# Optimization experiments

Hardware: AMD Instinct MI355X
Metric: run time of the kernel (lower is better)

## Reference

```python
import jax, jax.numpy as jnp
import numpy as np

B, C, IMG, P = 8, 6, 384, 16
DIM, HEADS, DEPTH, MLP, NCLS = 768, 12, 4, 3072, 1000
N = (IMG // P) ** 2            # 576 patches
DH = DIM // HEADS              # 64
PATCH_DIM = C * P * P          # 1536


def setup_inputs() -> dict:
    key = jax.random.key(0)
    ks = jax.random.split(key, 13)
    f = lambda k, shp, s=0.02: jax.random.normal(k, shp, jnp.float32) * s
    return {
        "x": jax.random.normal(ks[0], (B, C, IMG, IMG), jnp.float32),
        "patch_w": f(ks[1], (PATCH_DIM, DIM)),
        "patch_b": f(ks[2], (DIM,)),
        "ln1_g": jnp.ones((DEPTH, DIM), jnp.float32),
        "ln1_b": jnp.zeros((DEPTH, DIM), jnp.float32),
        "w_qkv": f(ks[3], (DEPTH, DIM, 3 * DIM)),
        "bias_att": f(ks[4], (DEPTH, HEADS, N, N), 0.5),
        "w_out": f(ks[5], (DEPTH, DIM, DIM)),
        "ln2_g": jnp.ones((DEPTH, DIM), jnp.float32),
        "ln2_b": jnp.zeros((DEPTH, DIM), jnp.float32),
        "w1": f(ks[6], (DEPTH, DIM, MLP)),
        "b1": f(ks[7], (DEPTH, MLP)),
        "w2": f(ks[8], (DEPTH, MLP, DIM)),
        "b2": f(ks[9], (DEPTH, DIM)),
        "lnh_g": jnp.ones((DIM,), jnp.float32),
        "lnh_b": jnp.zeros((DIM,), jnp.float32),
        "w_head": f(ks[10], (DIM, NCLS)),
        "b_head": f(ks[11], (NCLS,)),
    }


def _ln(x, g, b, eps=1e-5):
    m = x.mean(-1, keepdims=True)
    v = ((x - m) ** 2).mean(-1, keepdims=True)
    return (x - m) * jax.lax.rsqrt(v + eps) * g + b


def _patchify(x, patch_w, patch_b):
    # Rearrange 'b c (h p1) (w p2) -> b (h w) (p1 p2 c)' then Linear(patch_dim, dim)
    b = x.shape[0]
    g = IMG // P
    x = x.reshape(b, C, g, P, g, P).transpose(0, 2, 4, 3, 5, 1).reshape(b, g * g, PATCH_DIM)
    return x @ patch_w + patch_b


def _forward(x, patch_w, patch_b, ln1_g, ln1_b, w_qkv, bias_att, w_out,
             ln2_g, ln2_b, w1, b1, w2, b2, lnh_g, lnh_b, w_head, b_head):
    scale = DH ** -0.5
    tok = _patchify(x, patch_w, patch_b)  # [B, N, DIM]; pos_info='mul_att_normed' -> no pos_embed added

    def block(t, p):
        l1g, l1b, wqkv, bias, wout, l2g, l2b, ww1, bb1, ww2, bb2 = p
        h = _ln(t, l1g, l1b)
        qkv = h @ wqkv                                     # [B, N, 3*DIM]
        q, k, v = jnp.split(qkv, 3, axis=-1)
        rs = lambda a: a.reshape(t.shape[0], N, HEADS, DH).transpose(0, 2, 1, 3)
        q, k, v = rs(q), rs(k), rs(v)                      # [B, H, N, DH]
        dots = jnp.einsum('bhid,bhjd->bhij', q, k) * scale
        # mul_att_normed: softmax(qk) * softmax(bias), renormalized over keys
        attn = jax.nn.softmax(dots, axis=-1) * jax.nn.softmax(bias, axis=-1)[None]
        attn = attn / attn.sum(-1, keepdims=True)
        o = jnp.einsum('bhij,bhjd->bhid', attn, v)
        o = o.transpose(0, 2, 1, 3).reshape(t.shape[0], N, DIM) @ wout
        t = t + o
        h2 = _ln(t, l2g, l2b)
        t = t + (jax.nn.gelu(h2 @ ww1 + bb1, approximate=False) @ ww2 + bb2)
        return t, None

    tok, _ = jax.lax.scan(block, tok,
                          (ln1_g, ln1_b, w_qkv, bias_att, w_out,
                           ln2_g, ln2_b, w1, b1, w2, b2))
    pooled = tok.mean(axis=1)                              # mean-pool tokens
    return _ln(pooled, lnh_g, lnh_b) @ w_head + b_head     # [B, NCLS]


def reference(x, patch_w, patch_b, ln1_g, ln1_b, w_qkv, bias_att, w_out,
              ln2_g, ln2_b, w1, b1, w2, b2, lnh_g, lnh_b, w_head, b_head):
    return _forward(x, patch_w, patch_b, ln1_g, ln1_b, w_qkv, bias_att, w_out,
                    ln2_g, ln2_b, w1, b1, w2, b2, lnh_g, lnh_b, w_head, b_head)
```

## Files before the change

kernel.cpp:

```cpp
#include <hip/hip_runtime.h>
#include <hip/hip_bf16.h>

typedef __attribute__((ext_vector_type(8))) short bf16x8;
typedef __attribute__((ext_vector_type(4))) float f32x4;

#define DEVI __device__ __forceinline__

DEVI unsigned short f2bf_bits(float f) {
    __hip_bfloat16 h = __float2bfloat16(f);
    return *reinterpret_cast<unsigned short*>(&h);
}
DEVI float bfbits2f(unsigned short u) {
    __hip_bfloat16 h = *reinterpret_cast<__hip_bfloat16*>(&u);
    return __bfloat162float(h);
}

DEVI void gload_lds16(const void* g, void* lds) {
    __builtin_amdgcn_global_load_lds(
        (const __attribute__((address_space(1))) unsigned int*)g,
        (__attribute__((address_space(3))) unsigned int*)lds, 16, 0, 0);
}

template <int N> DEVI void wait_vm() {
    if constexpr (N == 0) asm volatile("s_waitcnt vmcnt(0)" ::: "memory");
    else if constexpr (N == 6) asm volatile("s_waitcnt vmcnt(6)" ::: "memory");
    else if constexpr (N == 12) asm volatile("s_waitcnt vmcnt(12)" ::: "memory");
    __builtin_amdgcn_sched_barrier(0);
}

DEVI int2 remap2d(int bid, int total, int gx) {
    int q = total >> 3, r = total & 7, x = bid & 7, l = bid >> 3;
    int seq = (x < r ? x * (q + 1) : r * (q + 1) + (x - r) * q) + l;
    int g4 = seq / (4 * gx);
    int rem = seq - g4 * 4 * gx;
    return {g4 * 4 + (rem & 3), rem >> 2};
}

__global__ __launch_bounds__(256) void patchify_kernel(const float* __restrict__ x,
                                                       unsigned short* __restrict__ patches)
{
    size_t t8 = (size_t)blockIdx.x * 256 + threadIdx.x;
    int jq = (int)(t8 % 48);
    size_t t = t8 / 48;
    int r = (int)(t % 384); t /= 384;
    int c = (int)(t % 6);
    int b = (int)(t / 6);
    int j = jq * 8;
    int gh = r >> 4, p1 = r & 15, gw = j >> 4, p2 = j & 15;
    int prow = b * 576 + gh * 24 + gw;
    int pcol = c * 256 + p1 * 16 + p2;
    const float* src = x + ((((size_t)b * 6 + c) * 384 + r) * 384 + j);
    float4 v0 = ((const float4*)src)[0];
    float4 v1 = ((const float4*)src)[1];
    ushort u[8] = { f2bf_bits(v0.x), f2bf_bits(v0.y), f2bf_bits(v0.z), f2bf_bits(v0.w),
                    f2bf_bits(v1.x), f2bf_bits(v1.y), f2bf_bits(v1.z), f2bf_bits(v1.w) };
    *(int4*)&patches[(size_t)prow * 1536 + pcol] = *(int4*)u;
}

__global__ __launch_bounds__(256) void convT_patch_kernel(const float* __restrict__ W,
                                                          __hip_bfloat16* __restrict__ Wt)
{
    __shared__ float tile[32][33];
    int n0 = blockIdx.x * 32, kp0 = blockIdx.y * 32;
    int tx = threadIdx.x & 31, ty = threadIdx.x >> 5;
#pragma unroll
    for (int i = 0; i < 4; i++) {
        int kp = kp0 + ty + 8 * i;
        int k = (kp & 255) * 6 + (kp >> 8);
        tile[ty + 8 * i][tx] = W[(size_t)k * 768 + n0 + tx];
    }
    __syncthreads();
#pragma unroll
    for (int i = 0; i < 4; i++)
        Wt[(size_t)(n0 + ty + 8 * i) * 1536 + kp0 + tx] = __float2bfloat16(tile[tx][ty + 8 * i]);
}

DEVI void convT_body(const float* __restrict__ W, __hip_bfloat16* __restrict__ Wt,
                     int K, int N, int k0, int n0, int tid)
{
    __shared__ float tile[32][33];
    int tx = tid & 31, ty = tid >> 5;
#pragma unroll
    for (int i = 0; i < 4; i++)
        tile[ty + 8 * i][tx] = W[(size_t)(k0 + ty + 8 * i) * N + n0 + tx];
    __syncthreads();
#pragma unroll
    for (int i = 0; i < 4; i++)
        Wt[(size_t)(n0 + ty + 8 * i) * K + k0 + tx] = __float2bfloat16(tile[tx][ty + 8 * i]);
}

__global__ __launch_bounds__(256) void convT4_kernel(const float* __restrict__ wqkv,
                                                     const float* __restrict__ wout,
                                                     const float* __restrict__ w1,
                                                     const float* __restrict__ w2,
                                                     __hip_bfloat16* __restrict__ dst)
{
    int bt = blockIdx.x;
    const float* W; __hip_bfloat16* Wt; int K, N, lt;
    if (bt < 1728)      { W = wqkv; K = 768;  N = 2304; lt = bt;        Wt = dst; }
    else if (bt < 2304) { W = wout; K = 768;  N = 768;  lt = bt - 1728; Wt = dst + 1769472; }
    else if (bt < 4608) { W = w1;   K = 768;  N = 3072; lt = bt - 2304; Wt = dst + 2359296; }
    else                { W = w2;   K = 3072; N = 768;  lt = bt - 4608; Wt = dst + 4718592; }
    int tn = N >> 5;
    convT_body(W, Wt, K, N, (lt / tn) * 32, (lt % tn) * 32, threadIdx.x);
}

DEVI float ld_ln(const float* p) { return *p; }
DEVI float ld_ln(const __hip_bfloat16* p) { return __bfloat162float(*p); }
DEVI void st_ln(float* p, float v) { *p = v; }
DEVI void st_ln(__hip_bfloat16* p, float v) { *p = __float2bfloat16(v); }

template <typename InT, typename OutT>
__global__ __launch_bounds__(256) void ln_kernel(const InT* __restrict__ x,
                                                 const float* __restrict__ g,
                                                 const float* __restrict__ b,
                                                 OutT* __restrict__ out)
{
    int row = blockIdx.x, tid = threadIdx.x;
    const InT* xr = x + (size_t)row * 768;
    float v0 = ld_ln(&xr[tid]), v1 = ld_ln(&xr[tid + 256]), v2 = ld_ln(&xr[tid + 512]);
    float s = v0 + v1 + v2;
    float s2 = v0 * v0 + v1 * v1 + v2 * v2;
#pragma unroll
    for (int m = 32; m >= 1; m >>= 1) { s += __shfl_xor(s, m); s2 += __shfl_xor(s2, m); }
    __shared__ float red[8];
    int w = tid >> 6;
    if ((tid & 63) == 0) { red[w] = s; red[4 + w] = s2; }
    __syncthreads();
    s = red[0] + red[1] + red[2] + red[3];
    s2 = red[4] + red[5] + red[6] + red[7];
    float mean = s * (1.0f / 768.0f);
    float var = s2 * (1.0f / 768.0f) - mean * mean;
    float rstd = rsqrtf(var + 1e-5f);
    OutT* orow = out + (size_t)row * 768;
    st_ln(&orow[tid], (v0 - mean) * rstd * g[tid] + b[tid]);
    st_ln(&orow[tid + 256], (v1 - mean) * rstd * g[tid + 256] + b[tid + 256]);
    st_ln(&orow[tid + 512], (v2 - mean) * rstd * g[tid + 512] + b[tid + 512]);
}

template <bool BIAS, bool RESID>
__global__ __launch_bounds__(256, 2) void gemm_bt_kernel(
    const __hip_bfloat16* __restrict__ A,
    const __hip_bfloat16* __restrict__ Bt,
    const float* __restrict__ bias,
    const __hip_bfloat16* __restrict__ resid,
    __hip_bfloat16* __restrict__ Cb,
    int M, int N, int K, int gx)
{
    constexpr int BM = 64, SL = 6;
    __shared__ __align__(16) __hip_bfloat16 As[3][BM * 64];
    __shared__ __align__(16) __hip_bfloat16 Bs[3][128 * 64];
    const int tid = threadIdx.x;
    const int wid = tid >> 6, lane = tid & 63;
    const int g = lane >> 4, l16 = lane & 15;
    const int wm = (wid >> 1) * 32, wn = (wid & 1) * 64;

    int2 bc = remap2d(blockIdx.x, gridDim.x, gx);
    const int bm = bc.x * BM, bn = bc.y * 128;

    const int sr32 = tid >> 3, ci = tid & 7;
    const int cg = ci ^ (sr32 & 7);
    const int sdst = tid * 8;
    size_t aOff[2], bOff[4];
#pragma unroll
    for (int i = 0; i < 2; i++) aOff[i] = (size_t)(bm + i * 32 + sr32) * K + cg * 8;
#pragma unroll
    for (int i = 0; i < 4; i++) bOff[i] = (size_t)(bn + i * 32 + sr32) * K + cg * 8;

    auto stage = [&](__hip_bfloat16* asb, __hip_bfloat16* bsb, int tq) {
        const __hip_bfloat16* ap = A + tq * 64;
        const __hip_bfloat16* bp = Bt + tq * 64;
#pragma unroll
        for (int i = 0; i < 2; i++) gload_lds16(ap + aOff[i], asb + i * 2048 + sdst);
#pragma unroll
        for (int i = 0; i < 4; i++) gload_lds16(bp + bOff[i], bsb + i * 2048 + sdst);
    };

    f32x4 acc[2][4] = {};
    const int nt = K >> 6;

    stage(As[0], Bs[0], 0);
    stage(As[1], Bs[1], 1);
    stage(As[2], Bs[2], 2);
    wait_vm<2 * SL>();
    __builtin_amdgcn_s_barrier();
    __builtin_amdgcn_sched_barrier(0);

    for (int t = 0; t < nt; t += 3) {
#pragma unroll
        for (int u = 0; u < 3; u++) {
            const int tc = t + u;
            bf16x8 af[2][2], bfr[2][4];
#pragma unroll
            for (int s = 0; s < 2; s++) {
                const int cp = ((s * 4 + g) ^ (l16 & 7)) << 3;
#pragma unroll
                for (int mi = 0; mi < 2; mi++)
                    af[s][mi] = *(const bf16x8*)&As[u][(wm + mi * 16 + l16) * 64 + cp];
#pragma unroll
                for (int ni = 0; ni < 4; ni++)
                    bfr[s][ni] = *(const bf16x8*)&Bs[u][(wn + ni * 16 + l16) * 64 + cp];
            }
#pragma unroll
            for (int s = 0; s < 2; s++)
#pragma unroll
                for (int mi = 0; mi < 2; mi++)
#pragma unroll
                    for (int ni = 0; ni < 4; ni++)
                        acc[mi][ni] = __builtin_amdgcn_mfma_f32_16x16x32_bf16(af[s][mi], bfr[s][ni], acc[mi][ni], 0, 0, 0);

            asm volatile("s_waitcnt lgkmcnt(0)" ::: "memory");
            __builtin_amdgcn_sched_barrier(0);
            __builtin_amdgcn_s_barrier();
            __builtin_amdgcn_sched_barrier(0);

            if (tc + 3 < nt) stage(As[u], Bs[u], tc + 3);
            if (tc + 1 < nt) {
                if (tc + 4 <= nt)      wait_vm<2 * SL>();
                else if (tc + 3 == nt) wait_vm<SL>();
                else                   wait_vm<0>();
                __builtin_amdgcn_s_barrier();
                __builtin_amdgcn_sched_barrier(0);
            }
        }
    }

    __hip_bfloat16* scr = &As[0][0] + wid * (16 * 72);
#pragma unroll
    for (int mi = 0; mi < 2; mi++) {
#pragma unroll
        for (int ni = 0; ni < 4; ni++) {
            float bval = 0.0f;
            if (BIAS) bval = bias[bn + wn + ni * 16 + l16];
#pragma unroll
            for (int r = 0; r < 4; r++)
                scr[(4 * g + r) * 72 + ni * 16 + l16] = __float2bfloat16(acc[mi][ni][r] + bval);
        }
        asm volatile("s_waitcnt lgkmcnt(0)" ::: "memory");
        __builtin_amdgcn_sched_barrier(0);
#pragma unroll
        for (int q2 = 0; q2 < 2; q2++) {
            int row16 = q2 * 8 + (lane >> 3), ch = lane & 7;
            bf16x8 vv = *(const bf16x8*)&scr[row16 * 72 + ch * 8];
            int grow = bm + wm + mi * 16 + row16;
            size_t off = (size_t)grow * N + bn + wn + ch * 8;
            if (RESID) {
                bf16x8 rv = *(const bf16x8*)&resid[off];
#pragma unroll
                for (int e = 0; e < 8; e++)
                    vv[e] = (short)f2bf_bits(bfbits2f((unsigned short)vv[e]) + bfbits2f((unsigned short)rv[e]));
            }
            *(int4*)&Cb[off] = *(int4*)&vv;
        }
        asm volatile("s_waitcnt lgkmcnt(0)" ::: "memory");
        __builtin_amdgcn_sched_barrier(0);
    }
}

template <bool BIAS, bool GELU>
__global__ __launch_bounds__(256, 2) void gemm_wide_kernel(
    const __hip_bfloat16* __restrict__ A,
    const __hip_bfloat16* __restrict__ Bt,
    const float* __restrict__ bias,
    __hip_bfloat16* __restrict__ Cb,
    int M, int N, int K, int gx)
{
    constexpr int SL = 6;
    __shared__ __align__(16) __hip_bfloat16 As[3][128 * 32];
    __shared__ __align__(16) __hip_bfloat16 Bs[3][256 * 32];
    const int tid = threadIdx.x;
    const int wid = tid >> 6, lane = tid & 63;
    const int g = lane >> 4, l16 = lane & 15;
    const int wm = (wid >> 1) * 64, wn = (wid & 1) * 128;

    int2 bc = remap2d(blockIdx.x, gridDim.x, gx);
    const int bm = bc.x * 128, bn = bc.y * 256;

    const int sr = tid >> 2;
    const int csrc = (lane & 3) ^ ((lane >> 3) & 3);
    const int sdst = sr * 32 + (lane & 3) * 8;
    size_t aOff[2], bOff[4];
#pragma unroll
    for (int i = 0; i < 2; i++) aOff[i] = (size_t)(bm + i * 64 + sr) * K + csrc * 8;
#pragma unroll
    for (int i = 0; i < 4; i++) bOff[i] = (size_t)(bn + i * 64 + sr) * K + csrc * 8;

    auto stage = [&](__hip_bfloat16* asb, __hip_bfloat16* bsb, int tq) {
        const __hip_bfloat16* ap = A + tq * 32;
        const __hip_bfloat16* bp = Bt + tq * 32;
#pragma unroll
        for (int i = 0; i < 2; i++) gload_lds16(ap + aOff[i], asb + i * 2048 + sdst);
#pragma unroll
        for (int i = 0; i < 4; i++) gload_lds16(bp + bOff[i], bsb + i * 2048 + sdst);
    };

    const int pSw = (l16 >> 1) & 3;
    f32x4 acc[4][8] = {};
    const int nt = K >> 5;

    stage(As[0], Bs[0], 0);
    stage(As[1], Bs[1], 1);
    stage(As[2], Bs[2], 2);
    wait_vm<2 * SL>();
    __builtin_amdgcn_s_barrier();
    __builtin_amdgcn_sched_barrier(0);

    for (int t = 0; t < nt; t += 3) {
#pragma unroll
        for (int u = 0; u < 3; u++) {
            const int tc = t + u;
            bf16x8 af[4], bfr[8];
#pragma unroll
            for (int mi = 0; mi < 4; mi++)
                af[mi] = *(const bf16x8*)&As[u][(wm + mi * 16 + l16) * 32 + ((g ^ pSw) << 3)];
#pragma unroll
            for (int ni = 0; ni < 8; ni++)
                bfr[ni] = *(const bf16x8*)&Bs[u][(wn + ni * 16 + l16) * 32 + ((g ^ pSw) << 3)];
#pragma unroll
            for (int mi = 0; mi < 4; mi++)
#pragma unroll
                for (int ni = 0; ni < 8; ni++)
                    acc[mi][ni] = __builtin_amdgcn_mfma_f32_16x16x32_bf16(af[mi], bfr[ni], acc[mi][ni], 0, 0, 0);

            asm volatile("s_waitcnt lgkmcnt(0)" ::: "memory");
            __builtin_amdgcn_sched_barrier(0);
            __builtin_amdgcn_s_barrier();
            __builtin_amdgcn_sched_barrier(0);

            if (tc + 3 < nt) stage(As[u], Bs[u], tc + 3);
            if (tc + 1 < nt) {
                if (tc + 4 <= nt)      wait_vm<2 * SL>();
                else if (tc + 3 == nt) wait_vm<SL>();
                else                   wait_vm<0>();
                __builtin_amdgcn_s_barrier();
                __builtin_amdgcn_sched_barrier(0);
            }
        }
    }

    __hip_bfloat16* scr = &As[0][0] + wid * (16 * 136);
#pragma unroll
    for (int mi = 0; mi < 4; mi++) {
#pragma unroll
        for (int ni = 0; ni < 8; ni++) {
            float bval = 0.0f;
            if (BIAS) bval = bias[bn + wn + ni * 16 + l16];
#pragma unroll
            for (int r = 0; r < 4; r++) {
                float v = acc[mi][ni][r] + bval;
                if (GELU) v = 0.5f * v * (1.0f + erff(v * 0.70710678118654752f));
                scr[(4 * g + r) * 136 + ni * 16 + l16] = __float2bfloat16(v);
            }
        }
        asm volatile("s_waitcnt lgkmcnt(0)" ::: "memory");
        __builtin_amdgcn_sched_barrier(0);
#pragma unroll
        for (int q2 = 0; q2 < 4; q2++) {
            int idx = q2 * 64 + lane;
            int row16 = idx >> 4, ch = idx & 15;
            bf16x8 vv = *(const bf16x8*)&scr[row16 * 136 + ch * 8];
            int grow = bm + wm + mi * 16 + row16;
            *(int4*)&Cb[(size_t)grow * N + bn + wn + ch * 8] = *(int4*)&vv;
        }
        asm volatile("s_waitcnt lgkmcnt(0)" ::: "memory");
        __builtin_amdgcn_sched_barrier(0);
    }
}

__global__ __launch_bounds__(256) void attn_kernel(const __hip_bfloat16* __restrict__ qkvb,
                                                   const float* __restrict__ bias,
                                                   unsigned short* __restrict__ o)
{
    const int seq = (blockIdx.x & 7) * 108 + (blockIdx.x >> 3);
    const int bb = seq & 7, qt = (seq >> 3) % 9, h = seq / 72;
    const int q0 = qt * 64;
    const int tid = threadIdx.x;
    const int wq = tid >> 6, lane = tid & 63, g = lane >> 4, l16 = lane & 15;

    __shared__ __align__(16) unsigned short Qs[64 * 72];
    __shared__ __align__(16) unsigned short Ks[64 * 72];
    __shared__ __align__(16) unsigned short Vt[64 * 72];
    __shared__ __align__(16) unsigned short Ps[4][16 * 72];

    {
        int r = tid >> 2, cb = (tid & 3) * 16;
        const int4* s4 = (const int4*)&qkvb[(size_t)(bb * 576 + q0 + r) * 2304 + h * 64 + cb];
        int4* d4 = (int4*)&Qs[r * 72 + cb];
        d4[0] = s4[0]; d4[1] = s4[1];
    }
    __syncthreads();
    bf16x8 qf0 = *(const bf16x8*)&Qs[(wq * 16 + l16) * 72 + g * 8];
    bf16x8 qf1 = *(const bf16x8*)&Qs[(wq * 16 + l16) * 72 + 32 + g * 8];

    float m_r[4] = {-1e30f, -1e30f, -1e30f, -1e30f};
    float l_r[4] = {0.f, 0.f, 0.f, 0.f};
    f32x4 oa[4] = {};
    const float* bias_h = bias + (size_t)h * 576 * 576;
    const float scale = 0.125f;

    for (int kt = 0; kt < 576; kt += 64) {
        {
            int r = tid >> 2, cb = (tid & 3) * 16;
            const int4* s4 = (const int4*)&qkvb[(size_t)(bb * 576 + kt + r) * 2304 + 768 + h * 64 + cb];
            int4* d4 = (int4*)&Ks[r * 72 + cb];
            d4[0] = s4[0]; d4[1] = s4[1];
            int key = tid & 63, d0 = (tid >> 6) * 16;
            const unsigned short* vs = (const unsigned short*)&qkvb[(size_t)(bb * 576 + kt + key) * 2304 + 1536 + h * 64 + d0];
            bf16x8 v0 = *(const bf16x8*)vs;
            bf16x8 v1 = *(const bf16x8*)(vs + 8);
#pragma unroll
            for (int e = 0; e < 8; e++) {
                Vt[(d0 + e) * 72 + key] = (unsigned short)v0[e];
                Vt[(d0 + 8 + e) * 72 + key] = (unsigned short)v1[e];
            }
        }
        __syncthreads();

        float bl[4][4];
#pragma unroll
        for (int kc = 0; kc < 4; kc++)
#pragma unroll
            for (int r = 0; r < 4; r++) {
                int q = q0 + wq * 16 + 4 * g + r;
                bl[kc][r] = bias_h[(size_t)q * 576 + kt + kc * 16 + l16];
            }

        f32x4 sc[4] = {};
        __builtin_amdgcn_s_setprio(1);
#pragma unroll
        for (int kc = 0; kc < 4; kc++) {
            bf16x8 kf0 = *(const bf16x8*)&Ks[(kc * 16 + l16) * 72 + g * 8];
            bf16x8 kf1 = *(const bf16x8*)&Ks[(kc * 16 + l16) * 72 + 32 + g * 8];
            sc[kc] = __builtin_amdgcn_mfma_f32_16x16x32_bf16(qf0, kf0, sc[kc], 0, 0, 0);
            sc[kc] = __builtin_amdgcn_mfma_f32_16x16x32_bf16(qf1, kf1, sc[kc], 0, 0, 0);
        }
        __builtin_amdgcn_s_setprio(0);

        float sv[4][4], mt[4] = {-1e30f, -1e30f, -1e30f, -1e30f};
#pragma unroll
        for (int kc = 0; kc < 4; kc++)
#pragma unroll
            for (int r = 0; r < 4; r++) {
                float s = sc[kc][r] * scale + bl[kc][r];
                sv[kc][r] = s;
                mt[r] = fmaxf(mt[r], s);
            }
#pragma unroll
        for (int r = 0; r < 4; r++)
#pragma unroll
            for (int m = 1; m < 16; m <<= 1) mt[r] = fmaxf(mt[r], __shfl_xor(mt[r], m));

        float sf[4];
#pragma unroll
        for (int r = 0; r < 4; r++) {
            float mn = fmaxf(m_r[r], mt[r]);
            sf[r] = __expf(m_r[r] - mn);
            m_r[r] = mn;
        }
        float rs[4] = {0.f, 0.f, 0.f, 0.f};
#pragma unroll
        for (int kc = 0; kc < 4; kc++)
#pragma unroll
            for (int r = 0; r < 4; r++) {
                float p = __expf(sv[kc][r] - m_r[r]);
                rs[r] += p;
                Ps[wq][(4 * g + r) * 72 + kc * 16 + l16] = f2bf_bits(p);
            }
#pragma unroll
        for (int r = 0; r < 4; r++) {
#pragma unroll
            for (int m = 1; m < 16; m <<= 1) rs[r] += __shfl_xor(rs[r], m);
            l_r[r] = l_r[r] * sf[r] + rs[r];
        }
#pragma unroll
        for (int dt = 0; dt < 4; dt++)
#pragma unroll
            for (int r = 0; r < 4; r++) oa[dt][r] *= sf[r];

        asm volatile("s_waitcnt lgkmcnt(0)" ::: "memory");

        __builtin_amdgcn_s_setprio(1);
#pragma unroll
        for (int s = 0; s < 2; s++) {
            bf16x8 pf = *(const bf16x8*)&Ps[wq][l16 * 72 + s * 32 + g * 8];
#pragma unroll
            for (int dt = 0; dt < 4; dt++) {
                bf16x8 vf = *(const bf16x8*)&Vt[(dt * 16 + l16) * 72 + s * 32 + g * 8];
                oa[dt] = __builtin_amdgcn_mfma_f32_16x16x32_bf16(pf, vf, oa[dt], 0, 0, 0);
            }
        }
        __builtin_amdgcn_s_setprio(0);
        __syncthreads();
    }

#pragma unroll
    for (int dt = 0; dt < 4; dt++)
#pragma unroll
        for (int r = 0; r < 4; r++) {
            int q = q0 + wq * 16 + 4 * g + r;
            float v = oa[dt][r] / l_r[r];
            o[(size_t)(bb * 576 + q) * 768 + h * 64 + dt * 16 + l16] = f2bf_bits(v);
        }
}

__global__ __launch_bounds__(256) void pool_kernel(const __hip_bfloat16* __restrict__ tok,
                                                   float* __restrict__ pooled)
{
    int d = blockIdx.x * 256 + threadIdx.x;
    int b = blockIdx.y;
    float s = 0.0f;
    for (int n = 0; n < 576; n++) s += __bfloat162float(tok[(size_t)(b * 576 + n) * 768 + d]);
    pooled[b * 768 + d] = s * (1.0f / 576.0f);
}

__global__ __launch_bounds__(256) void head_kernel(const float* __restrict__ lnp,
                                                   const float* __restrict__ w,
                                                   const float* __restrict__ bh,
                                                   float* __restrict__ out)
{
    int c = blockIdx.x * 256 + threadIdx.x;
    int b = blockIdx.y;
    if (c >= 1000) return;
    float s = bh[c];
    for (int d = 0; d < 768; d++) s += lnp[b * 768 + d] * w[(size_t)d * 1000 + c];
    out[b * 1000 + c] = s;
}

extern "C" void kernel_launch(void* const* d_in, const int* in_sizes, int n_in,
                              void* d_out, int out_size, void* d_ws, size_t ws_size,
                              hipStream_t stream)
{
    const float* x = (const float*)d_in[0];
    const float* patch_w = (const float*)d_in[1];
    const float* patch_b = (const float*)d_in[2];
    const float* ln1_g = (const float*)d_in[3];
    const float* ln1_b = (const float*)d_in[4];
    const float* w_qkv = (const float*)d_in[5];
    const float* bias_att = (const float*)d_in[6];
    const float* w_out = (const float*)d_in[7];
    const float* ln2_g = (const float*)d_in[8];
    const float* ln2_b = (const float*)d_in[9];
    const float* w1 = (const float*)d_in[10];
    const float* b1 = (const float*)d_in[11];
    const float* w2 = (const float*)d_in[12];
    const float* b2 = (const float*)d_in[13];
    const float* lnh_g = (const float*)d_in[14];
    const float* lnh_b = (const float*)d_in[15];
    const float* w_head = (const float*)d_in[16];
    const float* b_head = (const float*)d_in[17];
    float* out = (float*)d_out;

    char* ws = (char*)d_ws;
    __hip_bfloat16* tok = (__hip_bfloat16*)(ws + 0);
    __hip_bfloat16* qkv_bf = (__hip_bfloat16*)(ws + 14155776);
    float* pooled = (float*)(ws + 56623104);
    float* pooledln = (float*)(ws + 56647680);
    __hip_bfloat16* patches = (__hip_bfloat16*)(ws + 56672256);
    __hip_bfloat16* lw = patches;
    __hip_bfloat16* h_bf = (__hip_bfloat16*)(ws + 70828032);
    __hip_bfloat16* o_bf = (__hip_bfloat16*)(ws + 77905920);
    __hip_bfloat16* hid_bf = (__hip_bfloat16*)(ws + 84983808);
    __hip_bfloat16* wbuf = (__hip_bfloat16*)(ws + 113295360);

    patchify_kernel<<<3456, 256, 0, stream>>>(x, (unsigned short*)patches);
    convT_patch_kernel<<<dim3(24, 48), 256, 0, stream>>>(patch_w, wbuf);
    gemm_bt_kernel<true, false><<<432, 256, 0, stream>>>(
        patches, wbuf, patch_b, nullptr, tok, 4608, 768, 1536, 6);

    for (int l = 0; l < 4; l++) {
        convT4_kernel<<<6912, 256, 0, stream>>>(
            w_qkv + (size_t)l * 768 * 2304, w_out + (size_t)l * 768 * 768,
            w1 + (size_t)l * 768 * 3072, w2 + (size_t)l * 3072 * 768, lw);
        ln_kernel<__hip_bfloat16, __hip_bfloat16><<<4608, 256, 0, stream>>>(
            tok, ln1_g + l * 768, ln1_b + l * 768, h_bf);
        gemm_wide_kernel<false, false><<<324, 256, 0, stream>>>(
            h_bf, lw, nullptr, qkv_bf, 4608, 2304, 768, 9);
        attn_kernel<<<864, 256, 0, stream>>>(
            qkv_bf, bias_att + (size_t)l * 12 * 576 * 576, (unsigned short*)o_bf);
        gemm_bt_kernel<false, true><<<432, 256, 0, stream>>>(
            o_bf, lw + 1769472, nullptr, tok, tok, 4608, 768, 768, 6);
        ln_kernel<__hip_bfloat16, __hip_bfloat16><<<4608, 256, 0, stream>>>(
            tok, ln2_g + l * 768, ln2_b + l * 768, h_bf);
        gemm_wide_kernel<true, true><<<432, 256, 0, stream>>>(
            h_bf, lw + 2359296, b1 + l * 3072, hid_bf, 4608, 3072, 768, 12);
        gemm_bt_kernel<true, true><<<432, 256, 0, stream>>>(
            hid_bf, lw + 4718592, b2 + l * 768, tok, tok, 4608, 768, 3072, 6);
    }

    pool_kernel<<<dim3(3, 8), 256, 0, stream>>>(tok, pooled);
    ln_kernel<float, float><<<8, 256, 0, stream>>>(pooled, lnh_g, lnh_b, pooledln);
    head_kernel<<<dim3(4, 8), 256, 0, stream>>>(pooledln, w_head, b_head, out);
}
```

Measured before the change: 845.4 us.

## Replace wide GEMM with 64x128 tiles, batch weight conversion, vectorize LayerNorm

Removes the 128x256-tile wide GEMM and runs the QKV and MLP-up projections through the smaller 64x128 tile kernel, which gains a GELU template flag. The smaller tiles give more blocks (1296 and 1728) to fill the CUs, at the cost of less data reuse per block. When the workspace is large enough, all four layers' weights are transposed and converted in a single launch instead of one launch per layer. LayerNorm now runs 192 threads per row with float4/ushort4 vector loads and stores.

```diff
diff --git a/kernel.cpp b/kernel.cpp
--- a/kernel.cpp
+++ b/kernel.cpp
@@ -25,6 +25,10 @@
     if constexpr (N == 0) asm volatile("s_waitcnt vmcnt(0)" ::: "memory");
     else if constexpr (N == 6) asm volatile("s_waitcnt vmcnt(6)" ::: "memory");
     else if constexpr (N == 12) asm volatile("s_waitcnt vmcnt(12)" ::: "memory");
+    __builtin_amdgcn_sched_barrier(0);
+}
+DEVI void lgkm0() {
+    asm volatile("s_waitcnt lgkmcnt(0)" ::: "memory");
     __builtin_amdgcn_sched_barrier(0);
 }
 
@@ -89,56 +93,85 @@
         Wt[(size_t)(n0 + ty + 8 * i) * K + k0 + tx] = __float2bfloat16(tile[tx][ty + 8 * i]);
 }
 
-__global__ __launch_bounds__(256) void convT4_kernel(const float* __restrict__ wqkv,
-                                                     const float* __restrict__ wout,
-                                                     const float* __restrict__ w1,
-                                                     const float* __restrict__ w2,
-                                                     __hip_bfloat16* __restrict__ dst)
-{
-    int bt = blockIdx.x;
+DEVI void convT4_dispatch(int bt, const float* wqkv, const float* wout,
+                          const float* w1, const float* w2,
+                          __hip_bfloat16* dst, int tid)
+{
     const float* W; __hip_bfloat16* Wt; int K, N, lt;
     if (bt < 1728)      { W = wqkv; K = 768;  N = 2304; lt = bt;        Wt = dst; }
     else if (bt < 2304) { W = wout; K = 768;  N = 768;  lt = bt - 1728; Wt = dst + 1769472; }
     else if (bt < 4608) { W = w1;   K = 768;  N = 3072; lt = bt - 2304; Wt = dst + 2359296; }
     else                { W = w2;   K = 3072; N = 768;  lt = bt - 4608; Wt = dst + 4718592; }
     int tn = N >> 5;
-    convT_body(W, Wt, K, N, (lt / tn) * 32, (lt % tn) * 32, threadIdx.x);
-}
-
-DEVI float ld_ln(const float* p) { return *p; }
-DEVI float ld_ln(const __hip_bfloat16* p) { return __bfloat162float(*p); }
-DEVI void st_ln(float* p, float v) { *p = v; }
-DEVI void st_ln(__hip_bfloat16* p, float v) { *p = __float2bfloat16(v); }
+    convT_body(W, Wt, K, N, (lt / tn) * 32, (lt % tn) * 32, tid);
+}
+
+__global__ __launch_bounds__(256) void convT4_kernel(const float* __restrict__ wqkv,
+                                                     const float* __restrict__ wout,
+                                                     const float* __restrict__ w1,
+                                                     const float* __restrict__ w2,
+                                                     __hip_bfloat16* __restrict__ dst)
+{
+    convT4_dispatch(blockIdx.x, wqkv, wout, w1, w2, dst, threadIdx.x);
+}
+
+__global__ __launch_bounds__(256) void convT4all_kernel(const float* __restrict__ wqkv,
+                                                        const float* __restrict__ wout,
+                                                        const float* __restrict__ w1,
+                                                        const float* __restrict__ w2,
+                                                        __hip_bfloat16* __restrict__ dst)
+{
+    int l = blockIdx.x / 6912, bt = blockIdx.x % 6912;
+    convT4_dispatch(bt,
+                    wqkv + (size_t)l * 768 * 2304, wout + (size_t)l * 768 * 768,
+                    w1 + (size_t)l * 768 * 3072, w2 + (size_t)l * 3072 * 768,
+                    dst + (size_t)l * 7077888, threadIdx.x);
+}
+
+DEVI void ld4(const float* p, float* v) {
+    float4 t = *(const float4*)p; v[0] = t.x; v[1] = t.y; v[2] = t.z; v[3] = t.w;
+}
+DEVI void ld4(const __hip_bfloat16* p, float* v) {
+    ushort4 t = *(const ushort4*)p;
+    v[0] = bfbits2f(t.x); v[1] = bfbits2f(t.y); v[2] = bfbits2f(t.z); v[3] = bfbits2f(t.w);
+}
+DEVI void st4(float* p, const float* v) { *(float4*)p = make_float4(v[0], v[1], v[2], v[3]); }
+DEVI void st4(__hip_bfloat16* p, const float* v) {
+    ushort4 t = { f2bf_bits(v[0]), f2bf_bits(v[1]), f2bf_bits(v[2]), f2bf_bits(v[3]) };
+    *(ushort4*)p = t;
+}
 
 template <typename InT, typename OutT>
-__global__ __launch_bounds__(256) void ln_kernel(const InT* __restrict__ x,
+__global__ __launch_bounds__(192) void ln_kernel(const InT* __restrict__ x,
                                                  const float* __restrict__ g,
                                                  const float* __restrict__ b,
                                                  OutT* __restrict__ out)
 {
     int row = blockIdx.x, tid = threadIdx.x;
-    const InT* xr = x + (size_t)row * 768;
-    float v0 = ld_ln(&xr[tid]), v1 = ld_ln(&xr[tid + 256]), v2 = ld_ln(&xr[tid + 512]);
-    float s = v0 + v1 + v2;
-    float s2 = v0 * v0 + v1 * v1 + v2 * v2;
+    float v[4], gv[4], bv[4];
+    ld4(&x[(size_t)row * 768 + tid * 4], v);
+    float s = v[0] + v[1] + v[2] + v[3];
+    float s2 = v[0] * v[0] + v[1] * v[1] + v[2] * v[2] + v[3] * v[3];
 #pragma unroll
     for (int m = 32; m >= 1; m >>= 1) { s += __shfl_xor(s, m); s2 += __shfl_xor(s2, m); }
-    __shared__ float red[8];
+    __shared__ float red[6];
     int w = tid >> 6;
-    if ((tid & 63) == 0) { red[w] = s; red[4 + w] = s2; }
+    if ((tid & 63) == 0) { red[w] = s; red[3 + w] = s2; }
     __syncthreads();
-    s = red[0] + red[1] + red[2] + red[3];
-    s2 = red[4] + red[5] + red[6] + red[7];
+    s = red[0] + red[1] + red[2];
+    s2 = red[3] + red[4] + red[5];
     float mean = s * (1.0f / 768.0f);
     float var = s2 * (1.0f / 768.0f) - mean * mean;
     float rstd = rsqrtf(var + 1e-5f);
-    OutT* orow = out + (size_t)row * 768;
-    st_ln(&orow[tid], (v0 - mean) * rstd * g[tid] + b[tid]);
-    st_ln(&orow[tid + 256], (v1 - mean) * rstd * g[tid + 256] + b[tid + 256]);
-    st_ln(&orow[tid + 512], (v2 - mean) * rstd * g[tid + 512] + b[tid + 512]);
-}
-
-template <bool BIAS, bool RESID>
+    ld4(&g[tid * 4], gv);
+    ld4(&b[tid * 4], bv);
+    float o[4];
+#pragma unroll
+    for (int i = 0; i < 4; i++) o[i] = (v[i] - mean) * rstd * gv[i] + bv[i];
+    st4(&out[(size_t)row * 768 + tid * 4], o);
+}
+
+template <bool BIAS, bool RESID, bool GELU>
 __global__ __launch_bounds__(256, 2) void gemm_bt_kernel(
     const __hip_bfloat16* __restrict__ A,
     const __hip_bfloat16* __restrict__ Bt,
@@ -182,7 +215,7 @@
     stage(As[0], Bs[0], 0);
     stage(As[1], Bs[1], 1);
     stage(As[2], Bs[2], 2);
-    wait_vm<2 * SL>();
+    wait_vm<12>();
     __builtin_amdgcn_s_barrier();
     __builtin_amdgcn_sched_barrier(0);
 
@@ -209,15 +242,14 @@
                     for (int ni = 0; ni < 4; ni++)
                         acc[mi][ni] = __builtin_amdgcn_mfma_f32_16x16x32_bf16(af[s][mi], bfr[s][ni], acc[mi][ni], 0, 0, 0);
 
-            asm volatile("s_waitcnt lgkmcnt(0)" ::: "memory");
-            __builtin_amdgcn_sched_barrier(0);
+            lgkm0();
             __builtin_amdgcn_s_barrier();
             __builtin_amdgcn_sched_barrier(0);
 
             if (tc + 3 < nt) stage(As[u], Bs[u], tc + 3);
             if (tc + 1 < nt) {
-                if (tc + 4 <= nt)      wait_vm<2 * SL>();
-                else if (tc + 3 == nt) wait_vm<SL>();
+                if (tc + 4 <= nt)      wait_vm<12>();
+                else if (tc + 3 == nt) wait_vm<6>();
                 else                   wait_vm<0>();
                 __builtin_amdgcn_s_barrier();
                 __builtin_amdgcn_sched_barrier(0);
@@ -233,11 +265,13 @@
             float bval = 0.0f;
             if (BIAS) bval = bias[bn + wn + ni * 16 + l16];
 #pragma unroll
-            for (int r = 0; r < 4; r++)
-                scr[(4 * g + r) * 72 + ni * 16 + l16] = __float2bfloat16(acc[mi][ni][r] + bval);
-        }
-        asm volatile("s_waitcnt lgkmcnt(0)" ::: "memory");
-        __builtin_amdgcn_sched_barrier(0);
+            for (int r = 0; r < 4; r++) {
+                float v = acc[mi][ni][r] + bval;
+                if (GELU) v = 0.5f * v * (1.0f + erff(v * 0.70710678118654752f));
+                scr[(4 * g + r) * 72 + ni * 16 + l16] = __float2bfloat16(v);
+            }
+        }
+        lgkm0();
 #pragma unroll
         for (int q2 = 0; q2 < 2; q2++) {
             int row16 = q2 * 8 + (lane >> 3), ch = lane & 7;
@@ -252,118 +286,7 @@
             }
             *(int4*)&Cb[off] = *(int4*)&vv;
         }
-        asm volatile("s_waitcnt lgkmcnt(0)" ::: "memory");
-        __builtin_amdgcn_sched_barrier(0);
-    }
-}
-
-template <bool BIAS, bool GELU>
-__global__ __launch_bounds__(256, 2) void gemm_wide_kernel(
-    const __hip_bfloat16* __restrict__ A,
-    const __hip_bfloat16* __restrict__ Bt,
-    const float* __restrict__ bias,
-    __hip_bfloat16* __restrict__ Cb,
-    int M, int N, int K, int gx)
-{
-    constexpr int SL = 6;
-    __shared__ __align__(16) __hip_bfloat16 As[3][128 * 32];
-    __shared__ __align__(16) __hip_bfloat16 Bs[3][256 * 32];
-    const int tid = threadIdx.x;
-    const int wid = tid >> 6, lane = tid & 63;
-    const int g = lane >> 4, l16 = lane & 15;
-    const int wm = (wid >> 1) * 64, wn = (wid & 1) * 128;
-
-    int2 bc = remap2d(blockIdx.x, gridDim.x, gx);
-    const int bm = bc.x * 128, bn = bc.y * 256;
-
-    const int sr = tid >> 2;
-    const int csrc = (lane & 3) ^ ((lane >> 3) & 3);
-    const int sdst = sr * 32 + (lane & 3) * 8;
-    size_t aOff[2], bOff[4];
-#pragma unroll
-    for (int i = 0; i < 2; i++) aOff[i] = (size_t)(bm + i * 64 + sr) * K + csrc * 8;
-#pragma unroll
-    for (int i = 0; i < 4; i++) bOff[i] = (size_t)(bn + i * 64 + sr) * K + csrc * 8;
-
-    auto stage = [&](__hip_bfloat16* asb, __hip_bfloat16* bsb, int tq) {
-        const __hip_bfloat16* ap = A + tq * 32;
-        const __hip_bfloat16* bp = Bt + tq * 32;
-#pragma unroll
-        for (int i = 0; i < 2; i++) gload_lds16(ap + aOff[i], asb + i * 2048 + sdst);
-#pragma unroll
-        for (int i = 0; i < 4; i++) gload_lds16(bp + bOff[i], bsb + i * 2048 + sdst);
-    };
-
-    const int pSw = (l16 >> 1) & 3;
-    f32x4 acc[4][8] = {};
-    const int nt = K >> 5;
-
-    stage(As[0], Bs[0], 0);
-    stage(As[1], Bs[1], 1);
-    stage(As[2], Bs[2], 2);
-    wait_vm<2 * SL>();
-    __builtin_amdgcn_s_barrier();
-    __builtin_amdgcn_sched_barrier(0);
-
-    for (int t = 0; t < nt; t += 3) {
-#pragma unroll
-        for (int u = 0; u < 3; u++) {
-            const int tc = t + u;
-            bf16x8 af[4], bfr[8];
-#pragma unroll
-            for (int mi = 0; mi < 4; mi++)
-                af[mi] = *(const bf16x8*)&As[u][(wm + mi * 16 + l16) * 32 + ((g ^ pSw) << 3)];
-#pragma unroll
-            for (int ni = 0; ni < 8; ni++)
-                bfr[ni] = *(const bf16x8*)&Bs[u][(wn + ni * 16 + l16) * 32 + ((g ^ pSw) << 3)];
-#pragma unroll
-            for (int mi = 0; mi < 4; mi++)
-#pragma unroll
-                for (int ni = 0; ni < 8; ni++)
-                    acc[mi][ni] = __builtin_amdgcn_mfma_f32_16x16x32_bf16(af[mi], bfr[ni], acc[mi][ni], 0, 0, 0);
-
-            asm volatile("s_waitcnt lgkmcnt(0)" ::: "memory");
-            __builtin_amdgcn_sched_barrier(0);
-            __builtin_amdgcn_s_barrier();
-            __builtin_amdgcn_sched_barrier(0);
-
-            if (tc + 3 < nt) stage(As[u], Bs[u], tc + 3);
-            if (tc + 1 < nt) {
-                if (tc + 4 <= nt)      wait_vm<2 * SL>();
-                else if (tc + 3 == nt) wait_vm<SL>();
-                else                   wait_vm<0>();
-                __builtin_amdgcn_s_barrier();
-                __builtin_amdgcn_sched_barrier(0);
-            }
-        }
-    }
-
-    __hip_bfloat16* scr = &As[0][0] + wid * (16 * 136);
-#pragma unroll
-    for (int mi = 0; mi < 4; mi++) {
-#pragma unroll
-        for (int ni = 0; ni < 8; ni++) {
-            float bval = 0.0f;
-            if (BIAS) bval = bias[bn + wn + ni * 16 + l16];
-#pragma unroll
-            for (int r = 0; r < 4; r++) {
-                float v = acc[mi][ni][r] + bval;
-                if (GELU) v = 0.5f * v * (1.0f + erff(v * 0.70710678118654752f));
-                scr[(4 * g + r) * 136 + ni * 16 + l16] = __float2bfloat16(v);
-            }
-        }
-        asm volatile("s_waitcnt lgkmcnt(0)" ::: "memory");
-        __builtin_amdgcn_sched_barrier(0);
-#pragma unroll
-        for (int q2 = 0; q2 < 4; q2++) {
-            int idx = q2 * 64 + lane;
-            int row16 = idx >> 4, ch = idx & 15;
-            bf16x8 vv = *(const bf16x8*)&scr[row16 * 136 + ch * 8];
-            int grow = bm + wm + mi * 16 + row16;
-            *(int4*)&Cb[(size_t)grow * N + bn + wn + ch * 8] = *(int4*)&vv;
-        }
-        asm volatile("s_waitcnt lgkmcnt(0)" ::: "memory");
-        __builtin_amdgcn_sched_barrier(0);
+        lgkm0();
     }
 }
 
@@ -561,33 +484,40 @@
     __hip_bfloat16* o_bf = (__hip_bfloat16*)(ws + 77905920);
     __hip_bfloat16* hid_bf = (__hip_bfloat16*)(ws + 84983808);
     __hip_bfloat16* wbuf = (__hip_bfloat16*)(ws + 113295360);
+    __hip_bfloat16* lwAll = (__hip_bfloat16*)(ws + 118013952);
+    const bool useAll = ws_size >= (size_t)118013952 + 56623104;
 
     patchify_kernel<<<3456, 256, 0, stream>>>(x, (unsigned short*)patches);
     convT_patch_kernel<<<dim3(24, 48), 256, 0, stream>>>(patch_w, wbuf);
-    gemm_bt_kernel<true, false><<<432, 256, 0, stream>>>(
+    gemm_bt_kernel<true, false, false><<<432, 256, 0, stream>>>(
         patches, wbuf, patch_b, nullptr, tok, 4608, 768, 1536, 6);
 
+    if (useAll)
+        convT4all_kernel<<<27648, 256, 0, stream>>>(w_qkv, w_out, w1, w2, lwAll);
+
     for (int l = 0; l < 4; l++) {
-        convT4_kernel<<<6912, 256, 0, stream>>>(
-            w_qkv + (size_t)l * 768 * 2304, w_out + (size_t)l * 768 * 768,
-            w1 + (size_t)l * 768 * 3072, w2 + (size_t)l * 3072 * 768, lw);
-        ln_kernel<__hip_bfloat16, __hip_bfloat16><<<4608, 256, 0, stream>>>(
+        __hip_bfloat16* lwl = useAll ? lwAll + (size_t)l * 7077888 : lw;
+        if (!useAll)
+            convT4_kernel<<<6912, 256, 0, stream>>>(
+                w_qkv + (size_t)l * 768 * 2304, w_out + (size_t)l * 768 * 768,
+                w1 + (size_t)l * 768 * 3072, w2 + (size_t)l * 3072 * 768, lw);
+        ln_kernel<__hip_bfloat16, __hip_bfloat16><<<4608, 192, 0, stream>>>(
             tok, ln1_g + l * 768, ln1_b + l * 768, h_bf);
-        gemm_wide_kernel<false, false><<<324, 256, 0, stream>>>(
-            h_bf, lw, nullptr, qkv_bf, 4608, 2304, 768, 9);
+        gemm_bt_kernel<false, false, false><<<1296, 256, 0, stream>>>(
+            h_bf, lwl, nullptr, nullptr, qkv_bf, 4608, 2304, 768, 18);
         attn_kernel<<<864, 256, 0, stream>>>(
             qkv_bf, bias_att + (size_t)l * 12 * 576 * 576, (unsigned short*)o_bf);
-        gemm_bt_kernel<false, true><<<432, 256, 0, stream>>>(
-            o_bf, lw + 1769472, nullptr, tok, tok, 4608, 768, 768, 6);
-        ln_kernel<__hip_bfloat16, __hip_bfloat16><<<4608, 256, 0, stream>>>(
+        gemm_bt_kernel<false, true, false><<<432, 256, 0, stream>>>(
+            o_bf, lwl + 1769472, nullptr, tok, tok, 4608, 768, 768, 6);
+        ln_kernel<__hip_bfloat16, __hip_bfloat16><<<4608, 192, 0, stream>>>(
             tok, ln2_g + l * 768, ln2_b + l * 768, h_bf);
-        gemm_wide_kernel<true, true><<<432, 256, 0, stream>>>(
-            h_bf, lw + 2359296, b1 + l * 3072, hid_bf, 4608, 3072, 768, 12);
-        gemm_bt_kernel<true, true><<<432, 256, 0, stream>>>(
-            hid_bf, lw + 4718592, b2 + l * 768, tok, tok, 4608, 768, 3072, 6);
+        gemm_bt_kernel<true, false, true><<<1728, 256, 0, stream>>>(
+            h_bf, lwl + 2359296, b1 + l * 3072, nullptr, hid_bf, 4608, 3072, 768, 24);
+        gemm_bt_kernel<true, true, false><<<432, 256, 0, stream>>>(
+            hid_bf, lwl + 4718592, b2 + l * 768, tok, tok, 4608, 768, 3072, 6);
     }
 
     pool_kernel<<<dim3(3, 8), 256, 0, stream>>>(tok, pooled);
-    ln_kernel<float, float><<<8, 256, 0, stream>>>(pooled, lnh_g, lnh_b, pooledln);
+    ln_kernel<float, float><<<8, 192, 0, stream>>>(pooled, lnh_g, lnh_b, pooledln);
     head_kernel<<<dim3(4, 8), 256, 0, stream>>>(pooledln, w_head, b_head, out);
 }
```

Measured after the change: 905.7 us. 7.1% more time.
